# Kernel optimization log

Measured on AMD Instinct MI355X. Metric: run time of the kernel, lower is better.

The kernel has to match this reference:

```python
import jax, jax.numpy as jnp
import numpy as np

N = 50000      # nodes
E = 800000     # edges
C = 128        # feature width (in = hidden = out)
H = 2          # attention heads
ATT_SLOPE = 0.2   # GATConv leaky_relu slope
OUT_SLOPE = 0.01  # F.leaky_relu_ default slope


def setup_inputs() -> dict:
    key = jax.random.key(0)
    ks = jax.random.split(key, 12)
    s = 1.0 / np.sqrt(C)
    inp = {
        "x": jax.random.normal(ks[0], (N, C), jnp.float32),
        "edge_index": jax.random.randint(ks[1], (2, E), 0, N, dtype=jnp.int32),
        "edge_attr": jax.random.normal(ks[2], (E, C), jnp.float32),
        # GATConv layer 1 params (lin weight, att_src, att_dst, bias)
        "W1": jax.random.normal(ks[3], (C, H * C), jnp.float32) * s,
        "a_src1": jax.random.normal(ks[4], (H, C), jnp.float32) * s,
        "a_dst1": jax.random.normal(ks[5], (H, C), jnp.float32) * s,
        "b1": jnp.zeros((C,), jnp.float32),
        # GATConv layer 2 params
        "W2": jax.random.normal(ks[6], (C, H * C), jnp.float32) * s,
        "a_src2": jax.random.normal(ks[7], (H, C), jnp.float32) * s,
        "a_dst2": jax.random.normal(ks[8], (H, C), jnp.float32) * s,
        "b2": jnp.zeros((C,), jnp.float32),
    }
    return inp


def _segment_softmax(alpha, dst, n):
    # alpha: [E', H]; softmax over edges sharing the same dst node
    amax = jax.ops.segment_max(alpha, dst, num_segments=n)
    amax = jnp.where(jnp.isfinite(amax), amax, 0.0)
    ex = jnp.exp(alpha - amax[dst])
    denom = jax.ops.segment_sum(ex, dst, num_segments=n)
    return ex / (denom[dst] + 1e-16)


def _gat_layer(x, src, dst, W, a_s, a_d, b):
    # GATConv, concat=False (mean over heads), edge_dim=None, eval mode
    n = x.shape[0]
    xp = (x @ W).reshape(n, H, C)                  # [N,H,C]
    a_i = jnp.sum(xp * a_s, axis=-1)               # [N,H] src scores
    a_j = jnp.sum(xp * a_d, axis=-1)               # [N,H] dst scores
    e = jax.nn.leaky_relu(a_i[src] + a_j[dst], ATT_SLOPE)   # [E',H]
    att = _segment_softmax(e, dst, n)              # [E',H]
    msg = att[:, :, None] * xp[src]                # [E',H,C]
    out = jax.ops.segment_sum(msg, dst, num_segments=n)     # [N,H,C]
    return out.mean(axis=1) + b                    # concat=False -> mean heads


def reference(x, edge_index, edge_attr, W1, a_src1, a_dst1, b1,
              W2, a_src2, a_dst2, b2):
    src0, dst0 = edge_index[0], edge_index[1]
    loop = jnp.arange(x.shape[0], dtype=edge_index.dtype)
    src = jnp.concatenate([src0, loop])            # add self loops
    dst = jnp.concatenate([dst0, loop])
    score = None
    for (W, a_s, a_d, b) in ((W1, a_src1, a_dst1, b1),
                             (W2, a_src2, a_dst2, b2)):
        x = _gat_layer(x, src, dst, W, a_s, a_d, b)
        # edge score uses pre-activation x (leaky_relu_ happens after the gather)
        score = jnp.sum(x[src0] * x[dst0] * edge_attr, axis=-1)  # [E]
        x = jax.nn.leaky_relu(x, OUT_SLOPE)
        score = jax.nn.sigmoid(score)
    return x, score
```

## Files before the change

### kernel.cpp

```cpp
#include <hip/hip_runtime.h>
#include <hip/hip_bf16.h>

#define NN 50000
#define EE 800000
#define CC 128
#define HH 2
#define ATT_SLOPE 0.2f
#define OUT_SLOPE 0.01f

__device__ __forceinline__ float lrelu(float v, float s) {
    return v > 0.0f ? v : s * v;
}


__global__ void zero_kernel(int* __restrict__ p, int n) {
    int i = blockIdx.x * blockDim.x + threadIdx.x;
    if (i < n) p[i] = 0;
}

__global__ void count_kernel(const int* __restrict__ dst, int* __restrict__ cnt,
                             int E, int N) {
    int i = blockIdx.x * blockDim.x + threadIdx.x;
    int total = E + N;
    if (i >= total) return;
    int d = (i < E) ? dst[i] : (i - E);
    atomicAdd(&cnt[d], 1);
}

__global__ __launch_bounds__(256) void bsum_kernel(const int* __restrict__ cnt,
                                                   int* __restrict__ bsum, int n) {
    __shared__ int sh[4];
    int i = blockIdx.x * 256 + threadIdx.x;
    int v = (i < n) ? cnt[i] : 0;
    #pragma unroll
    for (int off = 32; off; off >>= 1) v += __shfl_xor(v, off);
    if ((threadIdx.x & 63) == 0) sh[threadIdx.x >> 6] = v;
    __syncthreads();
    if (threadIdx.x == 0) bsum[blockIdx.x] = sh[0] + sh[1] + sh[2] + sh[3];
}

__global__ __launch_bounds__(256) void bscan_kernel(int* __restrict__ bsum, int nb) {
    __shared__ int buf[2][256];
    int t = threadIdx.x;
    int v = (t < nb) ? bsum[t] : 0;
    buf[0][t] = v;
    __syncthreads();
    int cur = 0;
    for (int off = 1; off < 256; off <<= 1) {
        int nxt = cur ^ 1;
        int add = (t >= off) ? buf[cur][t - off] : 0;
        buf[nxt][t] = buf[cur][t] + add;
        __syncthreads();
        cur = nxt;
    }
    if (t < nb) bsum[t] = buf[cur][t] - v;
}

__global__ __launch_bounds__(256) void scan2_kernel(const int* __restrict__ cnt,
                                                    const int* __restrict__ boff,
                                                    int* __restrict__ rowptr,
                                                    int* __restrict__ fillptr, int n) {
    __shared__ int buf[2][256];
    int t = threadIdx.x;
    int i = blockIdx.x * 256 + t;
    int v = (i < n) ? cnt[i] : 0;
    buf[0][t] = v;
    __syncthreads();
    int cur = 0;
    for (int off = 1; off < 256; off <<= 1) {
        int nxt = cur ^ 1;
        int add = (t >= off) ? buf[cur][t - off] : 0;
        buf[nxt][t] = buf[cur][t] + add;
        __syncthreads();
        cur = nxt;
    }
    int excl = buf[cur][t] - v + boff[blockIdx.x];
    if (i < n) { rowptr[i] = excl; fillptr[i] = excl; }
    if (i == n - 1) rowptr[n] = excl + v;
}

__global__ void scatter_kernel(const int* __restrict__ src, const int* __restrict__ dst,
                               int* __restrict__ fillptr, int* __restrict__ col,
                               int E, int N) {
    int i = blockIdx.x * blockDim.x + threadIdx.x;
    int total = E + N;
    if (i >= total) return;
    int s, d;
    if (i < E) { s = src[i]; d = dst[i]; }
    else       { s = d = i - E; }
    int pos = atomicAdd(&fillptr[d], 1);
    col[pos] = s;
}


#define GSTEP(AC, BV) \
    acc[0][0] += a0.AC * BV.x; acc[0][1] += a0.AC * BV.y; acc[0][2] += a0.AC * BV.z; acc[0][3] += a0.AC * BV.w; \
    acc[1][0] += a1.AC * BV.x; acc[1][1] += a1.AC * BV.y; acc[1][2] += a1.AC * BV.z; acc[1][3] += a1.AC * BV.w; \
    acc[2][0] += a2.AC * BV.x; acc[2][1] += a2.AC * BV.y; acc[2][2] += a2.AC * BV.z; acc[2][3] += a2.AC * BV.w; \
    acc[3][0] += a3.AC * BV.x; acc[3][1] += a3.AC * BV.y; acc[3][2] += a3.AC * BV.z; acc[3][3] += a3.AC * BV.w;

__global__ __launch_bounds__(256) void gemm_kernel(const float* __restrict__ X,
                            const float* __restrict__ W,
                            const float* __restrict__ a_src,
                            const float* __restrict__ a_dst,
                            float* __restrict__ XP,
                            float* __restrict__ a4,
                            int M, float slope) {
    __shared__ float As[64][68];
    __shared__ float Bs[64][68];
    int m0 = blockIdx.x * 64;
    int n0 = blockIdx.y * 64;
    int t  = threadIdx.x;
    int tx = t & 15;
    int ty = t >> 4;

    float acc[4][4] = {};

    for (int kt = 0; kt < 2; ++kt) {
        #pragma unroll
        for (int j = 0; j < 4; ++j) {
            int idx = t + j * 256;
            int row = idx >> 4;
            int kq  = idx & 15;
            float4 v = make_float4(0.f, 0.f, 0.f, 0.f);
            if (m0 + row < M)
                v = *(const float4*)(X + (size_t)(m0 + row) * CC + kt * 64 + kq * 4);
            v.x = lrelu(v.x, slope); v.y = lrelu(v.y, slope);
            v.z = lrelu(v.z, slope); v.w = lrelu(v.w, slope);
            *(float4*)(&As[row][kq * 4]) = v;
        }
        #pragma unroll
        for (int j = 0; j < 4; ++j) {
            int idx = t + j * 256;
            int k   = idx >> 4;
            int cq  = idx & 15;
            *(float4*)(&Bs[k][cq * 4]) =
                *(const float4*)(W + (size_t)(kt * 64 + k) * 256 + n0 + cq * 4);
        }
        __syncthreads();
        #pragma unroll
        for (int k0 = 0; k0 < 64; k0 += 4) {
            float4 a0 = *(const float4*)(&As[ty * 4 + 0][k0]);
            float4 a1 = *(const float4*)(&As[ty * 4 + 1][k0]);
            float4 a2 = *(const float4*)(&As[ty * 4 + 2][k0]);
            float4 a3 = *(const float4*)(&As[ty * 4 + 3][k0]);
            float4 b0 = *(const float4*)(&Bs[k0 + 0][tx * 4]);
            float4 b1 = *(const float4*)(&Bs[k0 + 1][tx * 4]);
            float4 b2 = *(const float4*)(&Bs[k0 + 2][tx * 4]);
            float4 b3 = *(const float4*)(&Bs[k0 + 3][tx * 4]);
            GSTEP(x, b0);
            GSTEP(y, b1);
            GSTEP(z, b2);
            GSTEP(w, b3);
        }
        __syncthreads();
    }

    int h = n0 >> 7;
    int coff = (n0 & 127) + tx * 4;
    float4 asv = *(const float4*)(a_src + h * 128 + coff);
    float4 adv = *(const float4*)(a_dst + h * 128 + coff);
    #pragma unroll
    for (int i = 0; i < 4; ++i) {
        int row = m0 + ty * 4 + i;
        float4 o = make_float4(acc[i][0], acc[i][1], acc[i][2], acc[i][3]);
        float ps = o.x * asv.x + o.y * asv.y + o.z * asv.z + o.w * asv.w;
        float pd = o.x * adv.x + o.y * adv.y + o.z * adv.z + o.w * adv.w;
        #pragma unroll
        for (int off = 1; off < 16; off <<= 1) {
            ps += __shfl_xor(ps, off);
            pd += __shfl_xor(pd, off);
        }
        if (row < M) {
            *(float4*)(XP + (size_t)row * 256 + n0 + tx * 4) = o;
            if (tx == 0) {
                atomicAdd(&a4[(size_t)row * 4 + h], ps);
                atomicAdd(&a4[(size_t)row * 4 + 2 + h], pd);
            }
        }
    }
}

__global__ __launch_bounds__(256) void agg_kernel(const float* __restrict__ xp,
                           const float* __restrict__ a4,
                           const int* __restrict__ rowptr,
                           const int* __restrict__ col,
                           const float* __restrict__ bias,
                           float* __restrict__ out_pre) {
    int n = __builtin_amdgcn_readfirstlane(blockIdx.x * 4 + (int)(threadIdx.x >> 6));
    int lane = threadIdx.x & 63;
    int h = lane >> 5;
    int r0 = rowptr[n], r1 = rowptr[n + 1];
    float2 adv = *(const float2*)(a4 + (size_t)n * 4 + 2);
    float ad = h ? adv.y : adv.x;

    float denom = 0.f;
    float4 acc = make_float4(0.f, 0.f, 0.f, 0.f);

    int k = r0;
    for (; k + 3 < r1; k += 4) {
        int s0 = __builtin_amdgcn_readfirstlane(col[k]);
        int s1 = __builtin_amdgcn_readfirstlane(col[k + 1]);
        int s2 = __builtin_amdgcn_readfirstlane(col[k + 2]);
        int s3 = __builtin_amdgcn_readfirstlane(col[k + 3]);
        float2 av0 = *(const float2*)(a4 + (size_t)s0 * 4);
        float2 av1 = *(const float2*)(a4 + (size_t)s1 * 4);
        float2 av2 = *(const float2*)(a4 + (size_t)s2 * 4);
        float2 av3 = *(const float2*)(a4 + (size_t)s3 * 4);
        float4 v0 = *(const float4*)(xp + (size_t)s0 * 256 + lane * 4);
        float4 v1 = *(const float4*)(xp + (size_t)s1 * 256 + lane * 4);
        float4 v2 = *(const float4*)(xp + (size_t)s2 * 256 + lane * 4);
        float4 v3 = *(const float4*)(xp + (size_t)s3 * 256 + lane * 4);
        float e0 = lrelu((h ? av0.y : av0.x) + ad, ATT_SLOPE);
        float e1 = lrelu((h ? av1.y : av1.x) + ad, ATT_SLOPE);
        float e2 = lrelu((h ? av2.y : av2.x) + ad, ATT_SLOPE);
        float e3 = lrelu((h ? av3.y : av3.x) + ad, ATT_SLOPE);
        float x0 = __expf(e0);
        float x1 = __expf(e1);
        float x2 = __expf(e2);
        float x3 = __expf(e3);
        denom += (x0 + x1) + (x2 + x3);
        acc.x += x0 * v0.x + x1 * v1.x + x2 * v2.x + x3 * v3.x;
        acc.y += x0 * v0.y + x1 * v1.y + x2 * v2.y + x3 * v3.y;
        acc.z += x0 * v0.z + x1 * v1.z + x2 * v2.z + x3 * v3.z;
        acc.w += x0 * v0.w + x1 * v1.w + x2 * v2.w + x3 * v3.w;
    }
    for (; k < r1; ++k) {
        int s0 = __builtin_amdgcn_readfirstlane(col[k]);
        float2 av0 = *(const float2*)(a4 + (size_t)s0 * 4);
        float4 v0 = *(const float4*)(xp + (size_t)s0 * 256 + lane * 4);
        float e0 = lrelu((h ? av0.y : av0.x) + ad, ATT_SLOPE);
        float x0 = __expf(e0);
        denom += x0;
        acc.x += x0 * v0.x;
        acc.y += x0 * v0.y;
        acc.z += x0 * v0.z;
        acc.w += x0 * v0.w;
    }

    float inv = 1.0f / (denom + 1e-16f);
    float4 val = make_float4(acc.x * inv, acc.y * inv, acc.z * inv, acc.w * inv);
    float4 other;
    other.x = __shfl_xor(val.x, 32);
    other.y = __shfl_xor(val.y, 32);
    other.z = __shfl_xor(val.z, 32);
    other.w = __shfl_xor(val.w, 32);
    if (h == 0) {
        float4 bv = *(const float4*)(bias + lane * 4);
        float4 o;
        o.x = 0.5f * (val.x + other.x) + bv.x;
        o.y = 0.5f * (val.y + other.y) + bv.y;
        o.z = 0.5f * (val.z + other.z) + bv.z;
        o.w = 0.5f * (val.w + other.w) + bv.w;
        *(float4*)(out_pre + (size_t)n * CC + lane * 4) = o;
    }
}

__global__ __launch_bounds__(256) void score_kernel(const float* __restrict__ x2,
                             const int* __restrict__ src,
                             const int* __restrict__ dst,
                             const float* __restrict__ ea,
                             float* __restrict__ score) {
    int e = blockIdx.x * 8 + (int)(threadIdx.x >> 5);
    int q = threadIdx.x & 31;
    int s = src[e], d = dst[e];
    float4 xs = *(const float4*)(x2 + (size_t)s * CC + q * 4);
    float4 xd = *(const float4*)(x2 + (size_t)d * CC + q * 4);
    float4 ev = *(const float4*)(ea + (size_t)e * CC + q * 4);
    float p = xs.x * xd.x * ev.x + xs.y * xd.y * ev.y +
              xs.z * xd.z * ev.z + xs.w * xd.w * ev.w;
    #pragma unroll
    for (int off = 16; off; off >>= 1) p += __shfl_xor(p, off);
    if (q == 0) score[e] = 1.0f / (1.0f + __expf(-p));
}

__global__ void lrelu_kernel(float* __restrict__ x, int n4) {
    int i = blockIdx.x * blockDim.x + threadIdx.x;
    if (i >= n4) return;
    float4 v = ((float4*)x)[i];
    v.x = lrelu(v.x, OUT_SLOPE); v.y = lrelu(v.y, OUT_SLOPE);
    v.z = lrelu(v.z, OUT_SLOPE); v.w = lrelu(v.w, OUT_SLOPE);
    ((float4*)x)[i] = v;
}

extern "C" void kernel_launch(void* const* d_in, const int* in_sizes, int n_in,
                              void* d_out, int out_size, void* d_ws, size_t ws_size,
                              hipStream_t stream) {
    (void)in_sizes; (void)n_in; (void)out_size; (void)ws_size;
    const float* x       = (const float*)d_in[0];
    const int*   eidx    = (const int*)d_in[1];
    const float* ea      = (const float*)d_in[2];
    const float* W1      = (const float*)d_in[3];
    const float* a_src1  = (const float*)d_in[4];
    const float* a_dst1  = (const float*)d_in[5];
    const float* b1      = (const float*)d_in[6];
    const float* W2      = (const float*)d_in[7];
    const float* a_src2  = (const float*)d_in[8];
    const float* a_dst2  = (const float*)d_in[9];
    const float* b2      = (const float*)d_in[10];

    const int* srcp = eidx;
    const int* dstp = eidx + EE;

    char* ws = (char*)d_ws;
    auto alloc = [&](size_t bytes) {
        char* p = ws;
        ws += (bytes + 255) & ~(size_t)255;
        return p;
    };
    const int NB = (NN + 255) / 256;
    int*   cnt     = (int*)alloc((size_t)NN * 4);
    int*   rowptr  = (int*)alloc((size_t)(NN + 1) * 4);
    int*   fillptr = (int*)alloc((size_t)NN * 4);
    int*   col     = (int*)alloc((size_t)(EE + NN) * 4);
    int*   bsum    = (int*)alloc((size_t)NB * 4);
    float* a4      = (float*)alloc((size_t)NN * 4 * 4);
    float* xp      = (float*)alloc((size_t)NN * 256 * 4);
    float* x1      = (float*)alloc((size_t)NN * CC * 4);

    float* outx = (float*)d_out;
    float* outs = outx + (size_t)NN * CC;

    int total = EE + NN;

    zero_kernel<<<(NN + 255) / 256, 256, 0, stream>>>(cnt, NN);
    zero_kernel<<<(NN * 4 + 255) / 256, 256, 0, stream>>>((int*)a4, NN * 4);
    count_kernel<<<(total + 255) / 256, 256, 0, stream>>>(dstp, cnt, EE, NN);
    bsum_kernel<<<NB, 256, 0, stream>>>(cnt, bsum, NN);
    bscan_kernel<<<1, 256, 0, stream>>>(bsum, NB);
    scan2_kernel<<<NB, 256, 0, stream>>>(cnt, bsum, rowptr, fillptr, NN);
    scatter_kernel<<<(total + 255) / 256, 256, 0, stream>>>(srcp, dstp, fillptr, col, EE, NN);

    dim3 ggrid((NN + 63) / 64, 4);

    gemm_kernel<<<ggrid, 256, 0, stream>>>(x, W1, a_src1, a_dst1, xp, a4, NN, 1.0f);
    agg_kernel<<<NN / 4, 256, 0, stream>>>(xp, a4, rowptr, col, b1, x1);

    zero_kernel<<<(NN * 4 + 255) / 256, 256, 0, stream>>>((int*)a4, NN * 4);
    gemm_kernel<<<ggrid, 256, 0, stream>>>(x1, W2, a_src2, a_dst2, xp, a4, NN, OUT_SLOPE);
    agg_kernel<<<NN / 4, 256, 0, stream>>>(xp, a4, rowptr, col, b2, outx);

    score_kernel<<<EE / 8, 256, 0, stream>>>(outx, srcp, dstp, ea, outs);
    lrelu_kernel<<<((NN * CC / 4) + 255) / 256, 256, 0, stream>>>(outx, NN * CC / 4);
}
```

Measured before the change: 1.066 ms.

## Retile GEMM per head, fuse output leaky_relu into aggregation, drop atomics

The GEMM is retiled to 128x128 blocks, one per head, with an 8x8 micro-tile per thread. Because a whole head's columns now sit in one block, the attention scores are written directly instead of accumulated with atomics, and the a4 zeroing launches go away. The output leaky_relu moves into the aggregation epilogue and the separate lrelu kernel is removed. The score kernel recovers pre-activation values by inverting the leaky_relu (scaling negatives by 100), which adds a little rounding error in exchange for one fewer pass over the node features.

```diff
diff --git a/kernel.cpp b/kernel.cpp
--- a/kernel.cpp
+++ b/kernel.cpp
@@ -93,11 +93,12 @@
 }
 
 
-#define GSTEP(AC, BV) \
-    acc[0][0] += a0.AC * BV.x; acc[0][1] += a0.AC * BV.y; acc[0][2] += a0.AC * BV.z; acc[0][3] += a0.AC * BV.w; \
-    acc[1][0] += a1.AC * BV.x; acc[1][1] += a1.AC * BV.y; acc[1][2] += a1.AC * BV.z; acc[1][3] += a1.AC * BV.w; \
-    acc[2][0] += a2.AC * BV.x; acc[2][1] += a2.AC * BV.y; acc[2][2] += a2.AC * BV.z; acc[2][3] += a2.AC * BV.w; \
-    acc[3][0] += a3.AC * BV.x; acc[3][1] += a3.AC * BV.y; acc[3][2] += a3.AC * BV.z; acc[3][3] += a3.AC * BV.w;
+#define BM 128
+#define BK 32
+
+#define FMA8(i, ac, bb0, bb1) \
+    acc[i][0] += ac * bb0.x; acc[i][1] += ac * bb0.y; acc[i][2] += ac * bb0.z; acc[i][3] += ac * bb0.w; \
+    acc[i][4] += ac * bb1.x; acc[i][5] += ac * bb1.y; acc[i][6] += ac * bb1.z; acc[i][7] += ac * bb1.w;
 
 __global__ __launch_bounds__(256) void gemm_kernel(const float* __restrict__ X,
                             const float* __restrict__ W,
@@ -105,77 +106,82 @@
                             const float* __restrict__ a_dst,
                             float* __restrict__ XP,
                             float* __restrict__ a4,
-                            int M, float slope) {
-    __shared__ float As[64][68];
-    __shared__ float Bs[64][68];
-    int m0 = blockIdx.x * 64;
-    int n0 = blockIdx.y * 64;
+                            int M) {
+    __shared__ float As[BM][BK + 4];
+    __shared__ float Bs[BK][128 + 4];
+    int m0 = blockIdx.x * BM;
+    int h  = blockIdx.y;
+    int n0 = h << 7;
     int t  = threadIdx.x;
     int tx = t & 15;
     int ty = t >> 4;
 
-    float acc[4][4] = {};
-
-    for (int kt = 0; kt < 2; ++kt) {
+    float acc[8][8] = {};
+
+    for (int kt = 0; kt < CC; kt += BK) {
         #pragma unroll
         for (int j = 0; j < 4; ++j) {
             int idx = t + j * 256;
-            int row = idx >> 4;
-            int kq  = idx & 15;
+            int row = idx >> 3;
+            int kq  = idx & 7;
             float4 v = make_float4(0.f, 0.f, 0.f, 0.f);
             if (m0 + row < M)
-                v = *(const float4*)(X + (size_t)(m0 + row) * CC + kt * 64 + kq * 4);
-            v.x = lrelu(v.x, slope); v.y = lrelu(v.y, slope);
-            v.z = lrelu(v.z, slope); v.w = lrelu(v.w, slope);
+                v = *(const float4*)(X + (size_t)(m0 + row) * CC + kt + kq * 4);
             *(float4*)(&As[row][kq * 4]) = v;
         }
         #pragma unroll
         for (int j = 0; j < 4; ++j) {
             int idx = t + j * 256;
-            int k   = idx >> 4;
-            int cq  = idx & 15;
+            int k   = idx >> 5;
+            int cq  = idx & 31;
             *(float4*)(&Bs[k][cq * 4]) =
-                *(const float4*)(W + (size_t)(kt * 64 + k) * 256 + n0 + cq * 4);
+                *(const float4*)(W + (size_t)(kt + k) * 256 + n0 + cq * 4);
         }
         __syncthreads();
         #pragma unroll
-        for (int k0 = 0; k0 < 64; k0 += 4) {
-            float4 a0 = *(const float4*)(&As[ty * 4 + 0][k0]);
-            float4 a1 = *(const float4*)(&As[ty * 4 + 1][k0]);
-            float4 a2 = *(const float4*)(&As[ty * 4 + 2][k0]);
-            float4 a3 = *(const float4*)(&As[ty * 4 + 3][k0]);
-            float4 b0 = *(const float4*)(&Bs[k0 + 0][tx * 4]);
-            float4 b1 = *(const float4*)(&Bs[k0 + 1][tx * 4]);
-            float4 b2 = *(const float4*)(&Bs[k0 + 2][tx * 4]);
-            float4 b3 = *(const float4*)(&Bs[k0 + 3][tx * 4]);
-            GSTEP(x, b0);
-            GSTEP(y, b1);
-            GSTEP(z, b2);
-            GSTEP(w, b3);
+        for (int k0 = 0; k0 < BK; k0 += 4) {
+            float4 av[8];
+            #pragma unroll
+            for (int i = 0; i < 8; ++i)
+                av[i] = *(const float4*)(&As[ty * 8 + i][k0]);
+            #pragma unroll
+            for (int kk = 0; kk < 4; ++kk) {
+                float4 b0 = *(const float4*)(&Bs[k0 + kk][tx * 8]);
+                float4 b1 = *(const float4*)(&Bs[k0 + kk][tx * 8 + 4]);
+                if (kk == 0) { FMA8(0, av[0].x, b0, b1); FMA8(1, av[1].x, b0, b1); FMA8(2, av[2].x, b0, b1); FMA8(3, av[3].x, b0, b1); FMA8(4, av[4].x, b0, b1); FMA8(5, av[5].x, b0, b1); FMA8(6, av[6].x, b0, b1); FMA8(7, av[7].x, b0, b1); }
+                if (kk == 1) { FMA8(0, av[0].y, b0, b1); FMA8(1, av[1].y, b0, b1); FMA8(2, av[2].y, b0, b1); FMA8(3, av[3].y, b0, b1); FMA8(4, av[4].y, b0, b1); FMA8(5, av[5].y, b0, b1); FMA8(6, av[6].y, b0, b1); FMA8(7, av[7].y, b0, b1); }
+                if (kk == 2) { FMA8(0, av[0].z, b0, b1); FMA8(1, av[1].z, b0, b1); FMA8(2, av[2].z, b0, b1); FMA8(3, av[3].z, b0, b1); FMA8(4, av[4].z, b0, b1); FMA8(5, av[5].z, b0, b1); FMA8(6, av[6].z, b0, b1); FMA8(7, av[7].z, b0, b1); }
+                if (kk == 3) { FMA8(0, av[0].w, b0, b1); FMA8(1, av[1].w, b0, b1); FMA8(2, av[2].w, b0, b1); FMA8(3, av[3].w, b0, b1); FMA8(4, av[4].w, b0, b1); FMA8(5, av[5].w, b0, b1); FMA8(6, av[6].w, b0, b1); FMA8(7, av[7].w, b0, b1); }
+            }
         }
         __syncthreads();
     }
 
-    int h = n0 >> 7;
-    int coff = (n0 & 127) + tx * 4;
-    float4 asv = *(const float4*)(a_src + h * 128 + coff);
-    float4 adv = *(const float4*)(a_dst + h * 128 + coff);
+    int coff = tx * 8;
+    float4 as0 = *(const float4*)(a_src + h * 128 + coff);
+    float4 as1 = *(const float4*)(a_src + h * 128 + coff + 4);
+    float4 ad0 = *(const float4*)(a_dst + h * 128 + coff);
+    float4 ad1 = *(const float4*)(a_dst + h * 128 + coff + 4);
     #pragma unroll
-    for (int i = 0; i < 4; ++i) {
-        int row = m0 + ty * 4 + i;
-        float4 o = make_float4(acc[i][0], acc[i][1], acc[i][2], acc[i][3]);
-        float ps = o.x * asv.x + o.y * asv.y + o.z * asv.z + o.w * asv.w;
-        float pd = o.x * adv.x + o.y * adv.y + o.z * adv.z + o.w * adv.w;
+    for (int i = 0; i < 8; ++i) {
+        int row = m0 + ty * 8 + i;
+        float ps = acc[i][0] * as0.x + acc[i][1] * as0.y + acc[i][2] * as0.z + acc[i][3] * as0.w
+                 + acc[i][4] * as1.x + acc[i][5] * as1.y + acc[i][6] * as1.z + acc[i][7] * as1.w;
+        float pd = acc[i][0] * ad0.x + acc[i][1] * ad0.y + acc[i][2] * ad0.z + acc[i][3] * ad0.w
+                 + acc[i][4] * ad1.x + acc[i][5] * ad1.y + acc[i][6] * ad1.z + acc[i][7] * ad1.w;
         #pragma unroll
         for (int off = 1; off < 16; off <<= 1) {
             ps += __shfl_xor(ps, off);
             pd += __shfl_xor(pd, off);
         }
         if (row < M) {
-            *(float4*)(XP + (size_t)row * 256 + n0 + tx * 4) = o;
+            *(float4*)(XP + (size_t)row * 256 + n0 + tx * 8) =
+                make_float4(acc[i][0], acc[i][1], acc[i][2], acc[i][3]);
+            *(float4*)(XP + (size_t)row * 256 + n0 + tx * 8 + 4) =
+                make_float4(acc[i][4], acc[i][5], acc[i][6], acc[i][7]);
             if (tx == 0) {
-                atomicAdd(&a4[(size_t)row * 4 + h], ps);
-                atomicAdd(&a4[(size_t)row * 4 + 2 + h], pd);
+                a4[(size_t)row * 4 + h]     = ps;
+                a4[(size_t)row * 4 + 2 + h] = pd;
             }
         }
     }
@@ -186,7 +192,7 @@
                            const int* __restrict__ rowptr,
                            const int* __restrict__ col,
                            const float* __restrict__ bias,
-                           float* __restrict__ out_pre) {
+                           float* __restrict__ out_post) {
     int n = __builtin_amdgcn_readfirstlane(blockIdx.x * 4 + (int)(threadIdx.x >> 6));
     int lane = threadIdx.x & 63;
     int h = lane >> 5;
@@ -248,12 +254,16 @@
     if (h == 0) {
         float4 bv = *(const float4*)(bias + lane * 4);
         float4 o;
-        o.x = 0.5f * (val.x + other.x) + bv.x;
-        o.y = 0.5f * (val.y + other.y) + bv.y;
-        o.z = 0.5f * (val.z + other.z) + bv.z;
-        o.w = 0.5f * (val.w + other.w) + bv.w;
-        *(float4*)(out_pre + (size_t)n * CC + lane * 4) = o;
-    }
+        o.x = lrelu(0.5f * (val.x + other.x) + bv.x, OUT_SLOPE);
+        o.y = lrelu(0.5f * (val.y + other.y) + bv.y, OUT_SLOPE);
+        o.z = lrelu(0.5f * (val.z + other.z) + bv.z, OUT_SLOPE);
+        o.w = lrelu(0.5f * (val.w + other.w) + bv.w, OUT_SLOPE);
+        *(float4*)(out_post + (size_t)n * CC + lane * 4) = o;
+    }
+}
+
+__device__ __forceinline__ float recon(float v) {
+    return v < 0.0f ? v * 100.0f : v;
 }
 
 __global__ __launch_bounds__(256) void score_kernel(const float* __restrict__ x2,
@@ -267,20 +277,11 @@
     float4 xs = *(const float4*)(x2 + (size_t)s * CC + q * 4);
     float4 xd = *(const float4*)(x2 + (size_t)d * CC + q * 4);
     float4 ev = *(const float4*)(ea + (size_t)e * CC + q * 4);
-    float p = xs.x * xd.x * ev.x + xs.y * xd.y * ev.y +
-              xs.z * xd.z * ev.z + xs.w * xd.w * ev.w;
+    float p = recon(xs.x) * recon(xd.x) * ev.x + recon(xs.y) * recon(xd.y) * ev.y +
+              recon(xs.z) * recon(xd.z) * ev.z + recon(xs.w) * recon(xd.w) * ev.w;
     #pragma unroll
     for (int off = 16; off; off >>= 1) p += __shfl_xor(p, off);
     if (q == 0) score[e] = 1.0f / (1.0f + __expf(-p));
-}
-
-__global__ void lrelu_kernel(float* __restrict__ x, int n4) {
-    int i = blockIdx.x * blockDim.x + threadIdx.x;
-    if (i >= n4) return;
-    float4 v = ((float4*)x)[i];
-    v.x = lrelu(v.x, OUT_SLOPE); v.y = lrelu(v.y, OUT_SLOPE);
-    v.z = lrelu(v.z, OUT_SLOPE); v.w = lrelu(v.w, OUT_SLOPE);
-    ((float4*)x)[i] = v;
 }
 
 extern "C" void kernel_launch(void* const* d_in, const int* in_sizes, int n_in,
@@ -324,22 +325,19 @@
     int total = EE + NN;
 
     zero_kernel<<<(NN + 255) / 256, 256, 0, stream>>>(cnt, NN);
-    zero_kernel<<<(NN * 4 + 255) / 256, 256, 0, stream>>>((int*)a4, NN * 4);
     count_kernel<<<(total + 255) / 256, 256, 0, stream>>>(dstp, cnt, EE, NN);
     bsum_kernel<<<NB, 256, 0, stream>>>(cnt, bsum, NN);
     bscan_kernel<<<1, 256, 0, stream>>>(bsum, NB);
     scan2_kernel<<<NB, 256, 0, stream>>>(cnt, bsum, rowptr, fillptr, NN);
     scatter_kernel<<<(total + 255) / 256, 256, 0, stream>>>(srcp, dstp, fillptr, col, EE, NN);
 
-    dim3 ggrid((NN + 63) / 64, 4);
-
-    gemm_kernel<<<ggrid, 256, 0, stream>>>(x, W1, a_src1, a_dst1, xp, a4, NN, 1.0f);
+    dim3 ggrid((NN + BM - 1) / BM, 2);
+
+    gemm_kernel<<<ggrid, 256, 0, stream>>>(x, W1, a_src1, a_dst1, xp, a4, NN);
     agg_kernel<<<NN / 4, 256, 0, stream>>>(xp, a4, rowptr, col, b1, x1);
 
-    zero_kernel<<<(NN * 4 + 255) / 256, 256, 0, stream>>>((int*)a4, NN * 4);
-    gemm_kernel<<<ggrid, 256, 0, stream>>>(x1, W2, a_src2, a_dst2, xp, a4, NN, OUT_SLOPE);
+    gemm_kernel<<<ggrid, 256, 0, stream>>>(x1, W2, a_src2, a_dst2, xp, a4, NN);
     agg_kernel<<<NN / 4, 256, 0, stream>>>(xp, a4, rowptr, col, b2, outx);
 
     score_kernel<<<EE / 8, 256, 0, stream>>>(outx, srcp, dstp, ea, outs);
-    lrelu_kernel<<<((NN * CC / 4) + 255) / 256, 256, 0, stream>>>(outx, NN * CC / 4);
-}
+}
```

After: 1.067 ms. No clear change (+0.2%).
